# Optimization experiments

Measured on AMD Instinct MI355X. Metric: run time of the kernel, lower is better.

## Reference

```python
import jax, jax.numpy as jnp
import numpy as np

X_DIM = 512
Z_DIM = 16
HEADS = 8
DIM_HEAD = 64
INNER = HEADS * DIM_HEAD
EPS = 1e-5


def _layernorm(t, g, b):
    mu = jnp.mean(t, axis=-1, keepdims=True)
    var = jnp.mean(jnp.square(t - mu), axis=-1, keepdims=True)
    return (t - mu) * jax.lax.rsqrt(var + EPS) * g + b


def setup_inputs() -> dict:
    key = jax.random.key(0)
    ks = jax.random.split(key, 8)
    B, N = 4, 2048
    s_x = 1.0 / np.sqrt(X_DIM)
    s_z = 1.0 / np.sqrt(Z_DIM)
    s_i = 1.0 / np.sqrt(INNER)
    return {
        "x": jax.random.normal(ks[0], (B, N, X_DIM), dtype=jnp.float32),
        "z": jax.random.normal(ks[1], (B, 1, Z_DIM), dtype=jnp.float32),
        "ln_x_g": jnp.ones((X_DIM,), jnp.float32),
        "ln_x_b": jnp.zeros((X_DIM,), jnp.float32),
        "ln_z_g": jnp.ones((Z_DIM,), jnp.float32),
        "ln_z_b": jnp.zeros((Z_DIM,), jnp.float32),
        "Wq": jax.random.normal(ks[2], (X_DIM, INNER), jnp.float32) * s_x,
        "Wk": jax.random.normal(ks[3], (X_DIM, INNER), jnp.float32) * s_x,
        "Wv": jax.random.normal(ks[4], (X_DIM, INNER), jnp.float32) * s_x,
        "Wz": jax.random.normal(ks[5], (Z_DIM, 2 * X_DIM), jnp.float32) * s_z,
        "Wo": jax.random.normal(ks[6], (INNER, X_DIM), jnp.float32) * s_i,
        "bo": jnp.zeros((X_DIM,), jnp.float32),
    }


def reference(x, z, ln_x_g, ln_x_b, ln_z_g, ln_z_b, Wq, Wk, Wv, Wz, Wo, bo):
    scale = DIM_HEAD ** (-0.5)
    # z path: LN -> Linear -> SiLU -> split into FiLM scale/shift
    zp = jax.nn.silu(_layernorm(z, ln_z_g, ln_z_b) @ Wz)  # [B, 1, 2*x_dim]
    z1, z2 = jnp.split(zp, 2, axis=-1)
    x_mod = _layernorm(x, ln_x_g, ln_x_b) * z1 + z2       # [B, N, x_dim]
    B, N, _ = x.shape

    def heads(t):  # [B, N, inner] -> [B, h, N, d]
        return t.reshape(B, N, HEADS, DIM_HEAD).transpose(0, 2, 1, 3)

    q = heads(x_mod @ Wq)
    k = heads(x_mod @ Wk)
    v = heads(x_mod @ Wv)
    sim = jnp.einsum('bhid,bhjd->bhij', q, k) * scale
    attn = jax.nn.softmax(sim, axis=-1)
    out = jnp.einsum('bhij,bhjd->bhid', attn, v)           # [B, h, N, d]
    out = out.transpose(0, 2, 1, 3).reshape(B, N, INNER)
    return out @ Wo + bo
```

## Files before the change

kernel.cpp:

```cpp
#include <hip/hip_runtime.h>

#define XD 512
#define HEADS 8
#define DH 64
#define NSEQ 2048
#define NBATCH 4
#define NROWS (NBATCH*NSEQ)

#define SCALE_L2E 0.18033688011112042f
#define DEFER_THR 4.0f

typedef __attribute__((ext_vector_type(8))) short bf16x8;
typedef __attribute__((ext_vector_type(8))) unsigned short u16x8;
typedef __attribute__((ext_vector_type(4))) float f32x4;
typedef __attribute__((ext_vector_type(16))) float f32x16;

__device__ __forceinline__ unsigned short f2bf(float f) {
  union { float f; unsigned u; } v; v.f = f;
  return (unsigned short)((v.u + 0x7fffu + ((v.u >> 16) & 1u)) >> 16);
}

__device__ __forceinline__ float fexp2(float x) {
#if __has_builtin(__builtin_amdgcn_exp2f)
  return __builtin_amdgcn_exp2f(x);
#else
  return exp2f(x);
#endif
}

__device__ __forceinline__ unsigned cvt_pk_bf16(float lo, float hi) {
  unsigned r;
  asm("v_cvt_pk_bf16_f32 %0, %1, %2" : "=v"(r) : "v"(lo), "v"(hi));
  return r;
}

__device__ __forceinline__ void gload_lds16(const unsigned short* g, unsigned short* l) {
  __builtin_amdgcn_global_load_lds(
      (const __attribute__((address_space(1))) unsigned int*)g,
      (__attribute__((address_space(3))) unsigned int*)l, 16, 0, 0);
}

__global__ __launch_bounds__(256) void zpath_kernel(
    const float* __restrict__ z, const float* __restrict__ g, const float* __restrict__ b,
    const float* __restrict__ Wz, float* __restrict__ z12) {
  int bb = blockIdx.x;
  int t = threadIdx.x;
  float zv[16];
  float mean = 0.f;
#pragma unroll
  for (int i = 0; i < 16; ++i) { zv[i] = z[bb * 16 + i]; mean += zv[i]; }
  mean *= (1.f / 16.f);
  float var = 0.f;
#pragma unroll
  for (int i = 0; i < 16; ++i) { float d = zv[i] - mean; var += d * d; }
  var *= (1.f / 16.f);
  float rs = rsqrtf(var + 1e-5f);
  float zn[16];
#pragma unroll
  for (int i = 0; i < 16; ++i) zn[i] = (zv[i] - mean) * rs * g[i] + b[i];
  for (int c = t; c < 1024; c += 256) {
    float acc = 0.f;
#pragma unroll
    for (int i = 0; i < 16; ++i) acc += zn[i] * Wz[i * 1024 + c];
    float s = acc / (1.f + __expf(-acc));
    z12[bb * 1024 + c] = s;
  }
}

__global__ __launch_bounds__(256) void xmod_kernel(
    const float* __restrict__ x, const float* __restrict__ g, const float* __restrict__ b,
    const float* __restrict__ z12, unsigned short* __restrict__ xm) {
  int wave = threadIdx.x >> 6, lane = threadIdx.x & 63;
  int row = blockIdx.x * 4 + wave;
  const float* xr = x + (size_t)row * XD;
  float4 v0 = ((const float4*)xr)[lane * 2];
  float4 v1 = ((const float4*)xr)[lane * 2 + 1];
  float vv[8] = {v0.x, v0.y, v0.z, v0.w, v1.x, v1.y, v1.z, v1.w};
  float sum = 0.f, sq = 0.f;
#pragma unroll
  for (int i = 0; i < 8; ++i) { sum += vv[i]; sq += vv[i] * vv[i]; }
#pragma unroll
  for (int o = 32; o; o >>= 1) { sum += __shfl_xor(sum, o); sq += __shfl_xor(sq, o); }
  float mean = sum * (1.f / 512.f);
  float var = sq * (1.f / 512.f) - mean * mean;
  float rs = rsqrtf(var + 1e-5f);
  int bb = row >> 11;
  const float* zz = z12 + bb * 1024;
  int c0 = lane * 8;
  u16x8 o8;
#pragma unroll
  for (int i = 0; i < 8; ++i) {
    int c = c0 + i;
    float t = (vv[i] - mean) * rs * g[c] + b[c];
    t = t * zz[c] + zz[512 + c];
    o8[i] = f2bf(t);
  }
  *(u16x8*)(xm + (size_t)row * XD + c0) = o8;
}

__global__ __launch_bounds__(256) void wtrans4_kernel(
    const float* __restrict__ W0, const float* __restrict__ W1,
    const float* __restrict__ W2, const float* __restrict__ W3,
    unsigned short* __restrict__ dst) {
  __shared__ float tile[32][33];
  int blk = blockIdx.x;
  int w = blk >> 8;
  int t = blk & 255;
  int tn = t >> 4, tk = t & 15;
  const float* W = (w == 0) ? W0 : (w == 1) ? W1 : (w == 2) ? W2 : W3;
  int r = threadIdx.x >> 5, c = threadIdx.x & 31;
#pragma unroll
  for (int i = 0; i < 4; ++i)
    tile[r + 8 * i][c] = W[(size_t)(tk * 32 + r + 8 * i) * 512 + tn * 32 + c];
  __syncthreads();
  unsigned short* d = dst + (size_t)w * 262144;
#pragma unroll
  for (int i = 0; i < 4; ++i)
    d[(size_t)(tn * 32 + r + 8 * i) * 512 + tk * 32 + c] = f2bf(tile[c][r + 8 * i]);
}

__global__ __launch_bounds__(256, 2) void gemm_qkv_kernel(
    const unsigned short* __restrict__ A, const unsigned short* __restrict__ Wt,
    unsigned short* __restrict__ Qo, unsigned short* __restrict__ Ko,
    unsigned short* __restrict__ Vo) {
  __shared__ unsigned short Alds[128 * 64];
  __shared__ unsigned short Blds[128 * 64];
  int widx = threadIdx.x >> 6, lane = threadIdx.x & 63;
  int blk = blockIdx.x;
  int nt = blk % 12, mt = blk / 12;
  int blkM = mt * 128, blkN = nt * 128;
  int wr = widx >> 1, wc = widx & 1;
  int lr = lane & 15, lg = lane >> 4;
  int srow = lane >> 3, sc8 = lane & 7;

  f32x4 acc[4][4] = {};

  for (int kc = 0; kc < 512; kc += 64) {
#pragma unroll
    for (int i = 0; i < 4; ++i) {
      int rb = widx * 32 + i * 8;
      int row = rb + srow;
      int cs = (sc8 ^ (row & 7)) * 8;
      gload_lds16(A + (size_t)(blkM + row) * 512 + kc + cs, &Alds[rb * 64]);
      gload_lds16(Wt + (size_t)(blkN + row) * 512 + kc + cs, &Blds[rb * 64]);
    }
    __syncthreads();

#pragma unroll
    for (int kh = 0; kh < 2; ++kh) {
      bf16x8 bfr[4];
#pragma unroll
      for (int ni = 0; ni < 4; ++ni) {
        int brow = wc * 64 + ni * 16 + lr;
        bfr[ni] = *(const bf16x8*)&Blds[brow * 64 + (((kh * 4 + lg) ^ (brow & 7)) * 8)];
      }
#pragma unroll
      for (int mi = 0; mi < 4; ++mi) {
        int arow = wr * 64 + mi * 16 + lr;
        bf16x8 afr = *(const bf16x8*)&Alds[arow * 64 + (((kh * 4 + lg) ^ (arow & 7)) * 8)];
#pragma unroll
        for (int ni = 0; ni < 4; ++ni)
          acc[mi][ni] = __builtin_amdgcn_mfma_f32_16x16x32_bf16(afr, bfr[ni], acc[mi][ni], 0, 0, 0);
      }
    }
    __syncthreads();
  }

  int cg = blkN >> 9;
#pragma unroll
  for (int mi = 0; mi < 4; ++mi)
#pragma unroll
    for (int ni = 0; ni < 4; ++ni) {
      int col = blkN + wc * 64 + ni * 16 + lr;
      int c = col & 511;
#pragma unroll
      for (int j = 0; j < 4; ++j) {
        int row = blkM + wr * 64 + mi * 16 + lg * 4 + j;
        float v = acc[mi][ni][j];
        if (cg == 0) {
          Qo[(size_t)row * 512 + c] = f2bf(v * SCALE_L2E);
        } else if (cg == 1) {
          Ko[(size_t)row * 512 + c] = f2bf(v);
        } else {
          int bb = row >> 11, n = row & 2047, h = c >> 6, d = c & 63;
          int j4 = n & 15;
          int slot = (j4 & 3) | (((j4 >> 3) & 1) << 2) | (((j4 >> 2) & 1) << 3);
          int np = (n & ~15) | slot;
          Vo[(((size_t)(bb * HEADS + h) * DH + d) << 11) + np] = f2bf(v);
        }
      }
    }
}

__global__ __launch_bounds__(256, 2) void gemm_out_kernel(
    const unsigned short* __restrict__ A, const unsigned short* __restrict__ Wt,
    float* __restrict__ out, const float* __restrict__ bias) {
  __shared__ unsigned short Alds[128 * 64];
  __shared__ unsigned short Blds[64 * 64];
  int widx = threadIdx.x >> 6, lane = threadIdx.x & 63;
  int blk = blockIdx.x;
  int nt = blk & 7, mt = blk >> 3;
  int blkM = mt * 128, blkN = nt * 64;
  int wr = widx >> 1, wc = widx & 1;
  int lr = lane & 15, lg = lane >> 4;
  int srow = lane >> 3, sc8 = lane & 7;

  f32x4 acc[4][2] = {};

  for (int kc = 0; kc < 512; kc += 64) {
#pragma unroll
    for (int i = 0; i < 4; ++i) {
      int rb = widx * 32 + i * 8;
      int row = rb + srow;
      int cs = (sc8 ^ (row & 7)) * 8;
      gload_lds16(A + (size_t)(blkM + row) * 512 + kc + cs, &Alds[rb * 64]);
    }
#pragma unroll
    for (int i = 0; i < 2; ++i) {
      int rb = widx * 16 + i * 8;
      int row = rb + srow;
      int cs = (sc8 ^ (row & 7)) * 8;
      gload_lds16(Wt + (size_t)(blkN + row) * 512 + kc + cs, &Blds[rb * 64]);
    }
    __syncthreads();

#pragma unroll
    for (int kh = 0; kh < 2; ++kh) {
      bf16x8 bfr[2];
#pragma unroll
      for (int ni = 0; ni < 2; ++ni) {
        int brow = wc * 32 + ni * 16 + lr;
        bfr[ni] = *(const bf16x8*)&Blds[brow * 64 + (((kh * 4 + lg) ^ (brow & 7)) * 8)];
      }
#pragma unroll
      for (int mi = 0; mi < 4; ++mi) {
        int arow = wr * 64 + mi * 16 + lr;
        bf16x8 afr = *(const bf16x8*)&Alds[arow * 64 + (((kh * 4 + lg) ^ (arow & 7)) * 8)];
#pragma unroll
        for (int ni = 0; ni < 2; ++ni)
          acc[mi][ni] = __builtin_amdgcn_mfma_f32_16x16x32_bf16(afr, bfr[ni], acc[mi][ni], 0, 0, 0);
      }
    }
    __syncthreads();
  }

#pragma unroll
  for (int mi = 0; mi < 4; ++mi)
#pragma unroll
    for (int ni = 0; ni < 2; ++ni) {
      int col = blkN + wc * 32 + ni * 16 + lr;
#pragma unroll
      for (int j = 0; j < 4; ++j) {
        int row = blkM + wr * 64 + mi * 16 + lg * 4 + j;
        out[(size_t)row * 512 + col] = acc[mi][ni][j] + bias[col];
      }
    }
}


#define AKV 64
#define NCH_S 16

#define STAGE_S(s_, buf, kcc) do {                                        \
    _Pragma("unroll")                                                     \
    for (int i = 0; i < 2; ++i) {                                         \
      int rb = wq * 16 + i * 8;                                           \
      int row = rb + (lane >> 3);                                         \
      int cs = (lane & 7) ^ (row & 7);                                    \
      gload_lds16(Kg + (size_t)((kcc) + row) * 512 + cs * 8, KLDS(s_, buf) + rb * 64); \
      gload_lds16(Vg + (size_t)row * NSEQ + (kcc) + cs * 8, VLDS(s_, buf) + rb * 64);  \
    }                                                                     \
  } while (0)

#define PROCESS64(kb_, vb_) do {                                          \
    f32x16 s[2];                                                          \
    __builtin_amdgcn_s_setprio(1);                                        \
    _Pragma("unroll")                                                     \
    for (int kt = 0; kt < 2; ++kt) {                                      \
      int krow = kt * 32 + ql;                                            \
      f32x16 z = {};                                                      \
      _Pragma("unroll")                                                   \
      for (int ks = 0; ks < 4; ++ks) {                                    \
        bf16x8 kf = *(const bf16x8*)((kb_) + krow * 64 + (((ks * 2 + hi) ^ (krow & 7)) * 8)); \
        z = __builtin_amdgcn_mfma_f32_32x32x16_bf16(kf, qf[ks], z, 0, 0, 0); \
      }                                                                   \
      s[kt] = z;                                                          \
    }                                                                     \
    __builtin_amdgcn_s_setprio(0);                                        \
    float m8 = s[0][0];                                                   \
    _Pragma("unroll")                                                     \
    for (int i = 1; i < 16; ++i) m8 = fmaxf(m8, s[0][i]);                 \
    _Pragma("unroll")                                                     \
    for (int i = 0; i < 16; ++i) m8 = fmaxf(m8, s[1][i]);                 \
    m8 = fmaxf(m8, __shfl_xor(m8, 32));                                   \
    bool grow = (m8 > m0 + DEFER_THR);                                    \
    if (__any((int)grow)) {                                               \
      float mn = fmaxf(m0, m8);                                           \
      float al = fexp2(m0 - mn);                                          \
      m0 = mn; l0 *= al;                                                  \
      _Pragma("unroll")                                                   \
      for (int dt = 0; dt < 2; ++dt)                                      \
        _Pragma("unroll")                                                 \
        for (int j = 0; j < 16; ++j) o[dt][j] *= al;                      \
    }                                                                     \
    float p0[16], p1[16]; float rs = 0.f;                                 \
    _Pragma("unroll")                                                     \
    for (int i = 0; i < 16; ++i) { p0[i] = fexp2(s[0][i] - m0); rs += p0[i]; } \
    _Pragma("unroll")                                                     \
    for (int i = 0; i < 16; ++i) { p1[i] = fexp2(s[1][i] - m0); rs += p1[i]; } \
    rs += __shfl_xor(rs, 32);                                             \
    l0 += rs;                                                             \
    union { unsigned w[4]; bf16x8 v; } pf[4];                             \
    _Pragma("unroll")                                                     \
    for (int d2 = 0; d2 < 4; ++d2) {                                      \
      pf[0].w[d2] = cvt_pk_bf16(p0[2 * d2], p0[2 * d2 + 1]);              \
      pf[1].w[d2] = cvt_pk_bf16(p0[8 + 2 * d2], p0[8 + 2 * d2 + 1]);      \
      pf[2].w[d2] = cvt_pk_bf16(p1[2 * d2], p1[2 * d2 + 1]);              \
      pf[3].w[d2] = cvt_pk_bf16(p1[8 + 2 * d2], p1[8 + 2 * d2 + 1]);      \
    }                                                                     \
    __builtin_amdgcn_s_setprio(1);                                        \
    _Pragma("unroll")                                                     \
    for (int dt = 0; dt < 2; ++dt) {                                      \
      int vrow = dt * 32 + ql;                                            \
      f32x16 acc = o[dt];                                                 \
      _Pragma("unroll")                                                   \
      for (int g = 0; g < 4; ++g) {                                       \
        bf16x8 vf = *(const bf16x8*)((vb_) + vrow * 64 + (((g * 2 + hi) ^ (vrow & 7)) * 8)); \
        acc = __builtin_amdgcn_mfma_f32_32x32x16_bf16(vf, pf[g].v, acc, 0, 0, 0); \
      }                                                                   \
      o[dt] = acc;                                                        \
    }                                                                     \
    __builtin_amdgcn_s_setprio(0);                                        \
  } while (0)

__global__ __launch_bounds__(512, 4) void attn_kernel(
    const unsigned short* __restrict__ Q, const unsigned short* __restrict__ K,
    const unsigned short* __restrict__ VT, unsigned short* __restrict__ O) {
  __shared__ __align__(16) unsigned short SH[2][2][2][64 * 64];
#define KLDS(s_, bf) (&SH[0][s_][bf][0])
#define VLDS(s_, bf) (&SH[1][s_][bf][0])
  int tid = threadIdx.x;
  int widx = tid >> 6, lane = tid & 63;
  int strm = widx >> 2;
  int wq = widx & 3;
  int blk = blockIdx.x;
  int xcd = blk & 7;
  int idx = blk >> 3;
  int bh = xcd * 4 + (idx >> 4);
  int qg = idx & 15;
  int b = bh >> 3, h = bh & 7;
  int ql = lane & 31, hi = lane >> 5;
  int qrow0 = qg * 128 + wq * 32;

  bf16x8 qf[4];
  const unsigned short* Qp = Q + (size_t)(b * NSEQ + qrow0 + ql) * 512 + h * 64 + hi * 8;
#pragma unroll
  for (int ks = 0; ks < 4; ++ks) qf[ks] = *(const bf16x8*)(Qp + ks * 16);

  const unsigned short* Kg = K + (size_t)b * NSEQ * 512 + h * 64 + (size_t)strm * 1024 * 512;
  const unsigned short* Vg = VT + (size_t)bh * DH * NSEQ + strm * 1024;

  float m0 = -3.0e38f, l0 = 0.f;
  f32x16 o[2] = {};

  STAGE_S(strm, 0, 0);
  __syncthreads();
  int cur = 0;
  for (int t = 0; t < NCH_S; ++t) {
    if (t + 1 < NCH_S) STAGE_S(strm, cur ^ 1, (t + 1) * AKV);
    const unsigned short* kb_ = KLDS(strm, cur);
    const unsigned short* vb_ = VLDS(strm, cur);
    PROCESS64(kb_, vb_);
    __syncthreads();
    cur ^= 1;
  }

  float* sm = (float*)&SH[0][0][0][0];
  if (strm == 1) {
    int base = (wq * 64 + lane) * 34;
    sm[base] = m0;
    sm[base + 1] = l0;
#pragma unroll
    for (int j = 0; j < 16; ++j) { sm[base + 2 + j] = o[0][j]; sm[base + 18 + j] = o[1][j]; }
  }
  __syncthreads();
  if (strm == 0) {
    int base = (wq * 64 + lane) * 34;
    float mB = sm[base], lB = sm[base + 1];
    float mN = fmaxf(m0, mB);
    float aA = fexp2(m0 - mN), aB = fexp2(mB - mN);
    float inv = 1.f / (l0 * aA + lB * aB);
    float aAi = aA * inv, aBi = aB * inv;
    size_t rowb = (size_t)(b * NSEQ + qrow0 + ql) * 512 + h * 64 + hi * 4;
#pragma unroll
    for (int dt = 0; dt < 2; ++dt)
#pragma unroll
      for (int c = 0; c < 8; ++c) {
        float vlo = o[dt][2 * c] * aAi + sm[base + 2 + dt * 16 + 2 * c] * aBi;
        float vhi = o[dt][2 * c + 1] * aAi + sm[base + 2 + dt * 16 + 2 * c + 1] * aBi;
        unsigned w = cvt_pk_bf16(vlo, vhi);
        int d0 = dt * 32 + 8 * (c >> 1) + (c & 1) * 2;
        *(unsigned*)(O + rowb + d0) = w;
      }
  }
}

extern "C" void kernel_launch(void* const* d_in, const int* in_sizes, int n_in,
                              void* d_out, int out_size, void* d_ws, size_t ws_size,
                              hipStream_t stream) {
  const float* x   = (const float*)d_in[0];
  const float* z   = (const float*)d_in[1];
  const float* lxg = (const float*)d_in[2];
  const float* lxb = (const float*)d_in[3];
  const float* lzg = (const float*)d_in[4];
  const float* lzb = (const float*)d_in[5];
  const float* Wq  = (const float*)d_in[6];
  const float* Wk  = (const float*)d_in[7];
  const float* Wv  = (const float*)d_in[8];
  const float* Wz  = (const float*)d_in[9];
  const float* Wo  = (const float*)d_in[10];
  const float* bo  = (const float*)d_in[11];

  char* ws = (char*)d_ws;
  unsigned short* xm  = (unsigned short*)(ws);
  unsigned short* qb  = (unsigned short*)(ws + 8388608);
  unsigned short* kb  = (unsigned short*)(ws + 16777216);
  unsigned short* vt  = (unsigned short*)(ws + 25165824);
  unsigned short* ao  = (unsigned short*)(ws + 33554432);
  unsigned short* wqt = (unsigned short*)(ws + 41943040);
  unsigned short* wot = (unsigned short*)(ws + 43515904);
  float*          z12 = (float*)(ws + 44040192);

  zpath_kernel<<<NBATCH, 256, 0, stream>>>(z, lzg, lzb, Wz, z12);
  xmod_kernel<<<NROWS / 4, 256, 0, stream>>>(x, lxg, lxb, z12, xm);
  wtrans4_kernel<<<1024, 256, 0, stream>>>(Wq, Wk, Wv, Wo, wqt);
  gemm_qkv_kernel<<<768, 256, 0, stream>>>(xm, wqt, qb, kb, vt);
  attn_kernel<<<512, 512, 0, stream>>>(qb, kb, vt, ao);
  gemm_out_kernel<<<512, 256, 0, stream>>>(ao, wot, (float*)d_out, bo);
}
```

Measured before the change: 106.0 us.

## Double-buffer GEMM LDS loads, merge z-path into weight transpose, tree-reduce softmax max

```diff
diff --git a/kernel.cpp b/kernel.cpp
--- a/kernel.cpp
+++ b/kernel.cpp
@@ -40,30 +40,51 @@
       (__attribute__((address_space(3))) unsigned int*)l, 16, 0, 0);
 }
 
-__global__ __launch_bounds__(256) void zpath_kernel(
-    const float* __restrict__ z, const float* __restrict__ g, const float* __restrict__ b,
+__global__ __launch_bounds__(256) void wtrans4z_kernel(
+    const float* __restrict__ W0, const float* __restrict__ W1,
+    const float* __restrict__ W2, const float* __restrict__ W3,
+    unsigned short* __restrict__ dst,
+    const float* __restrict__ z, const float* __restrict__ zg, const float* __restrict__ zb,
     const float* __restrict__ Wz, float* __restrict__ z12) {
-  int bb = blockIdx.x;
-  int t = threadIdx.x;
-  float zv[16];
-  float mean = 0.f;
-#pragma unroll
-  for (int i = 0; i < 16; ++i) { zv[i] = z[bb * 16 + i]; mean += zv[i]; }
-  mean *= (1.f / 16.f);
-  float var = 0.f;
-#pragma unroll
-  for (int i = 0; i < 16; ++i) { float d = zv[i] - mean; var += d * d; }
-  var *= (1.f / 16.f);
-  float rs = rsqrtf(var + 1e-5f);
-  float zn[16];
-#pragma unroll
-  for (int i = 0; i < 16; ++i) zn[i] = (zv[i] - mean) * rs * g[i] + b[i];
-  for (int c = t; c < 1024; c += 256) {
-    float acc = 0.f;
-#pragma unroll
-    for (int i = 0; i < 16; ++i) acc += zn[i] * Wz[i * 1024 + c];
-    float s = acc / (1.f + __expf(-acc));
-    z12[bb * 1024 + c] = s;
+  __shared__ float tile[32][33];
+  int blk = blockIdx.x;
+  if (blk < 1024) {
+    int w = blk >> 8;
+    int t = blk & 255;
+    int tn = t >> 4, tk = t & 15;
+    const float* W = (w == 0) ? W0 : (w == 1) ? W1 : (w == 2) ? W2 : W3;
+    int r = threadIdx.x >> 5, c = threadIdx.x & 31;
+#pragma unroll
+    for (int i = 0; i < 4; ++i)
+      tile[r + 8 * i][c] = W[(size_t)(tk * 32 + r + 8 * i) * 512 + tn * 32 + c];
+    __syncthreads();
+    unsigned short* d = dst + (size_t)w * 262144;
+#pragma unroll
+    for (int i = 0; i < 4; ++i)
+      d[(size_t)(tn * 32 + r + 8 * i) * 512 + tk * 32 + c] = f2bf(tile[c][r + 8 * i]);
+  } else {
+    int bb = blk - 1024;
+    int t = threadIdx.x;
+    float zv[16];
+    float mean = 0.f;
+#pragma unroll
+    for (int i = 0; i < 16; ++i) { zv[i] = z[bb * 16 + i]; mean += zv[i]; }
+    mean *= (1.f / 16.f);
+    float var = 0.f;
+#pragma unroll
+    for (int i = 0; i < 16; ++i) { float d = zv[i] - mean; var += d * d; }
+    var *= (1.f / 16.f);
+    float rs = rsqrtf(var + 1e-5f);
+    float zn[16];
+#pragma unroll
+    for (int i = 0; i < 16; ++i) zn[i] = (zv[i] - mean) * rs * zg[i] + zb[i];
+    for (int c = t; c < 1024; c += 256) {
+      float acc = 0.f;
+#pragma unroll
+      for (int i = 0; i < 16; ++i) acc += zn[i] * Wz[i * 1024 + c];
+      float s = acc / (1.f + __expf(-acc));
+      z12[bb * 1024 + c] = s;
+    }
   }
 }
 
@@ -98,33 +119,12 @@
   *(u16x8*)(xm + (size_t)row * XD + c0) = o8;
 }
 
-__global__ __launch_bounds__(256) void wtrans4_kernel(
-    const float* __restrict__ W0, const float* __restrict__ W1,
-    const float* __restrict__ W2, const float* __restrict__ W3,
-    unsigned short* __restrict__ dst) {
-  __shared__ float tile[32][33];
-  int blk = blockIdx.x;
-  int w = blk >> 8;
-  int t = blk & 255;
-  int tn = t >> 4, tk = t & 15;
-  const float* W = (w == 0) ? W0 : (w == 1) ? W1 : (w == 2) ? W2 : W3;
-  int r = threadIdx.x >> 5, c = threadIdx.x & 31;
-#pragma unroll
-  for (int i = 0; i < 4; ++i)
-    tile[r + 8 * i][c] = W[(size_t)(tk * 32 + r + 8 * i) * 512 + tn * 32 + c];
-  __syncthreads();
-  unsigned short* d = dst + (size_t)w * 262144;
-#pragma unroll
-  for (int i = 0; i < 4; ++i)
-    d[(size_t)(tn * 32 + r + 8 * i) * 512 + tk * 32 + c] = f2bf(tile[c][r + 8 * i]);
-}
-
 __global__ __launch_bounds__(256, 2) void gemm_qkv_kernel(
     const unsigned short* __restrict__ A, const unsigned short* __restrict__ Wt,
     unsigned short* __restrict__ Qo, unsigned short* __restrict__ Ko,
     unsigned short* __restrict__ Vo) {
-  __shared__ unsigned short Alds[128 * 64];
-  __shared__ unsigned short Blds[128 * 64];
+  __shared__ unsigned short Alds[2][128 * 64];
+  __shared__ unsigned short Blds[2][128 * 64];
   int widx = threadIdx.x >> 6, lane = threadIdx.x & 63;
   int blk = blockIdx.x;
   int nt = blk % 12, mt = blk / 12;
@@ -133,18 +133,25 @@
   int lr = lane & 15, lg = lane >> 4;
   int srow = lane >> 3, sc8 = lane & 7;
 
+#define STAGEQ(bf, kcc) do {                                              \
+    _Pragma("unroll")                                                     \
+    for (int i = 0; i < 4; ++i) {                                         \
+      int rb = widx * 32 + i * 8;                                         \
+      int row = rb + srow;                                                \
+      int cs = (sc8 ^ (row & 7)) * 8;                                     \
+      gload_lds16(A + (size_t)(blkM + row) * 512 + (kcc) + cs, &Alds[bf][rb * 64]);  \
+      gload_lds16(Wt + (size_t)(blkN + row) * 512 + (kcc) + cs, &Blds[bf][rb * 64]); \
+    }                                                                     \
+  } while (0)
+
   f32x4 acc[4][4] = {};
 
+  STAGEQ(0, 0);
+  asm volatile("s_waitcnt vmcnt(0)" ::: "memory");
+  __builtin_amdgcn_s_barrier();
+  int cur = 0;
   for (int kc = 0; kc < 512; kc += 64) {
-#pragma unroll
-    for (int i = 0; i < 4; ++i) {
-      int rb = widx * 32 + i * 8;
-      int row = rb + srow;
-      int cs = (sc8 ^ (row & 7)) * 8;
-      gload_lds16(A + (size_t)(blkM + row) * 512 + kc + cs, &Alds[rb * 64]);
-      gload_lds16(Wt + (size_t)(blkN + row) * 512 + kc + cs, &Blds[rb * 64]);
-    }
-    __syncthreads();
+    if (kc + 64 < 512) STAGEQ(cur ^ 1, kc + 64);
 
 #pragma unroll
     for (int kh = 0; kh < 2; ++kh) {
@@ -152,18 +159,20 @@
 #pragma unroll
       for (int ni = 0; ni < 4; ++ni) {
         int brow = wc * 64 + ni * 16 + lr;
-        bfr[ni] = *(const bf16x8*)&Blds[brow * 64 + (((kh * 4 + lg) ^ (brow & 7)) * 8)];
+        bfr[ni] = *(const bf16x8*)&Blds[cur][brow * 64 + (((kh * 4 + lg) ^ (brow & 7)) * 8)];
       }
 #pragma unroll
       for (int mi = 0; mi < 4; ++mi) {
         int arow = wr * 64 + mi * 16 + lr;
-        bf16x8 afr = *(const bf16x8*)&Alds[arow * 64 + (((kh * 4 + lg) ^ (arow & 7)) * 8)];
+        bf16x8 afr = *(const bf16x8*)&Alds[cur][arow * 64 + (((kh * 4 + lg) ^ (arow & 7)) * 8)];
 #pragma unroll
         for (int ni = 0; ni < 4; ++ni)
           acc[mi][ni] = __builtin_amdgcn_mfma_f32_16x16x32_bf16(afr, bfr[ni], acc[mi][ni], 0, 0, 0);
       }
     }
-    __syncthreads();
+    asm volatile("s_waitcnt vmcnt(0)" ::: "memory");
+    __builtin_amdgcn_s_barrier();
+    cur ^= 1;
   }
 
   int cg = blkN >> 9;
@@ -195,8 +204,8 @@
 __global__ __launch_bounds__(256, 2) void gemm_out_kernel(
     const unsigned short* __restrict__ A, const unsigned short* __restrict__ Wt,
     float* __restrict__ out, const float* __restrict__ bias) {
-  __shared__ unsigned short Alds[128 * 64];
-  __shared__ unsigned short Blds[64 * 64];
+  __shared__ unsigned short Alds[2][128 * 64];
+  __shared__ unsigned short Blds[2][64 * 64];
   int widx = threadIdx.x >> 6, lane = threadIdx.x & 63;
   int blk = blockIdx.x;
   int nt = blk & 7, mt = blk >> 3;
@@ -205,24 +214,31 @@
   int lr = lane & 15, lg = lane >> 4;
   int srow = lane >> 3, sc8 = lane & 7;
 
+#define STAGEO(bf, kcc) do {                                              \
+    _Pragma("unroll")                                                     \
+    for (int i = 0; i < 4; ++i) {                                         \
+      int rb = widx * 32 + i * 8;                                         \
+      int row = rb + srow;                                                \
+      int cs = (sc8 ^ (row & 7)) * 8;                                     \
+      gload_lds16(A + (size_t)(blkM + row) * 512 + (kcc) + cs, &Alds[bf][rb * 64]);  \
+    }                                                                     \
+    _Pragma("unroll")                                                     \
+    for (int i = 0; i < 2; ++i) {                                         \
+      int rb = widx * 16 + i * 8;                                         \
+      int row = rb + srow;                                                \
+      int cs = (sc8 ^ (row & 7)) * 8;                                     \
+      gload_lds16(Wt + (size_t)(blkN + row) * 512 + (kcc) + cs, &Blds[bf][rb * 64]); \
+    }                                                                     \
+  } while (0)
+
   f32x4 acc[4][2] = {};
 
+  STAGEO(0, 0);
+  asm volatile("s_waitcnt vmcnt(0)" ::: "memory");
+  __builtin_amdgcn_s_barrier();
+  int cur = 0;
   for (int kc = 0; kc < 512; kc += 64) {
-#pragma unroll
-    for (int i = 0; i < 4; ++i) {
-      int rb = widx * 32 + i * 8;
-      int row = rb + srow;
-      int cs = (sc8 ^ (row & 7)) * 8;
-      gload_lds16(A + (size_t)(blkM + row) * 512 + kc + cs, &Alds[rb * 64]);
-    }
-#pragma unroll
-    for (int i = 0; i < 2; ++i) {
-      int rb = widx * 16 + i * 8;
-      int row = rb + srow;
-      int cs = (sc8 ^ (row & 7)) * 8;
-      gload_lds16(Wt + (size_t)(blkN + row) * 512 + kc + cs, &Blds[rb * 64]);
-    }
-    __syncthreads();
+    if (kc + 64 < 512) STAGEO(cur ^ 1, kc + 64);
 
 #pragma unroll
     for (int kh = 0; kh < 2; ++kh) {
@@ -230,18 +246,20 @@
 #pragma unroll
       for (int ni = 0; ni < 2; ++ni) {
         int brow = wc * 32 + ni * 16 + lr;
-        bfr[ni] = *(const bf16x8*)&Blds[brow * 64 + (((kh * 4 + lg) ^ (brow & 7)) * 8)];
+        bfr[ni] = *(const bf16x8*)&Blds[cur][brow * 64 + (((kh * 4 + lg) ^ (brow & 7)) * 8)];
       }
 #pragma unroll
       for (int mi = 0; mi < 4; ++mi) {
         int arow = wr * 64 + mi * 16 + lr;
-        bf16x8 afr = *(const bf16x8*)&Alds[arow * 64 + (((kh * 4 + lg) ^ (arow & 7)) * 8)];
+        bf16x8 afr = *(const bf16x8*)&Alds[cur][arow * 64 + (((kh * 4 + lg) ^ (arow & 7)) * 8)];
 #pragma unroll
         for (int ni = 0; ni < 2; ++ni)
           acc[mi][ni] = __builtin_amdgcn_mfma_f32_16x16x32_bf16(afr, bfr[ni], acc[mi][ni], 0, 0, 0);
       }
     }
-    __syncthreads();
+    asm volatile("s_waitcnt vmcnt(0)" ::: "memory");
+    __builtin_amdgcn_s_barrier();
+    cur ^= 1;
   }
 
 #pragma unroll
@@ -287,11 +305,13 @@
       s[kt] = z;                                                          \
     }                                                                     \
     __builtin_amdgcn_s_setprio(0);                                        \
-    float m8 = s[0][0];                                                   \
-    _Pragma("unroll")                                                     \
-    for (int i = 1; i < 16; ++i) m8 = fmaxf(m8, s[0][i]);                 \
-    _Pragma("unroll")                                                     \
-    for (int i = 0; i < 16; ++i) m8 = fmaxf(m8, s[1][i]);                 \
+                                \
+    float q4[8];                                                          \
+    _Pragma("unroll")                                                     \
+    for (int i = 0; i < 8; ++i)                                           \
+      q4[i] = fmaxf(fmaxf(s[0][i], s[0][i + 8]), fmaxf(s[1][i], s[1][i + 8])); \
+    float m8 = fmaxf(fmaxf(fmaxf(q4[0], q4[1]), fmaxf(q4[2], q4[3])),     \
+                     fmaxf(fmaxf(q4[4], q4[5]), fmaxf(q4[6], q4[7])));    \
     m8 = fmaxf(m8, __shfl_xor(m8, 32));                                   \
     bool grow = (m8 > m0 + DEFER_THR);                                    \
     if (__any((int)grow)) {                                               \
@@ -303,11 +323,12 @@
         _Pragma("unroll")                                                 \
         for (int j = 0; j < 16; ++j) o[dt][j] *= al;                      \
     }                                                                     \
-    float p0[16], p1[16]; float rs = 0.f;                                 \
-    _Pragma("unroll")                                                     \
-    for (int i = 0; i < 16; ++i) { p0[i] = fexp2(s[0][i] - m0); rs += p0[i]; } \
-    _Pragma("unroll")                                                     \
-    for (int i = 0; i < 16; ++i) { p1[i] = fexp2(s[1][i] - m0); rs += p1[i]; } \
+    float p0[16], p1[16]; float rsA = 0.f, rsB = 0.f;                     \
+    _Pragma("unroll")                                                     \
+    for (int i = 0; i < 16; ++i) { p0[i] = fexp2(s[0][i] - m0); rsA += p0[i]; } \
+    _Pragma("unroll")                                                     \
+    for (int i = 0; i < 16; ++i) { p1[i] = fexp2(s[1][i] - m0); rsB += p1[i]; } \
+    float rs = rsA + rsB;                                                 \
     rs += __shfl_xor(rs, 32);                                             \
     l0 += rs;                                                             \
     union { unsigned w[4]; bf16x8 v; } pf[4];                             \
@@ -431,9 +452,8 @@
   unsigned short* wot = (unsigned short*)(ws + 43515904);
   float*          z12 = (float*)(ws + 44040192);
 
-  zpath_kernel<<<NBATCH, 256, 0, stream>>>(z, lzg, lzb, Wz, z12);
+  wtrans4z_kernel<<<1028, 256, 0, stream>>>(Wq, Wk, Wv, Wo, wqt, z, lzg, lzb, Wz, z12);
   xmod_kernel<<<NROWS / 4, 256, 0, stream>>>(x, lxg, lxb, z12, xm);
-  wtrans4_kernel<<<1024, 256, 0, stream>>>(Wq, Wk, Wv, Wo, wqt);
   gemm_qkv_kernel<<<768, 256, 0, stream>>>(xm, wqt, qb, kb, vt);
   attn_kernel<<<512, 512, 0, stream>>>(qb, kb, vt, ao);
   gemm_out_kernel<<<512, 256, 0, stream>>>(ao, wot, (float*)d_out, bo);
```

Result: slower. 115.2 us (+8.7%).

## Merge z-path into weight transpose, remap GEMM blocks per XCD, shorten softmax reductions

Applied to the files above, without the earlier changes.

```diff
diff --git a/kernel.cpp b/kernel.cpp
--- a/kernel.cpp
+++ b/kernel.cpp
@@ -40,30 +40,51 @@
       (__attribute__((address_space(3))) unsigned int*)l, 16, 0, 0);
 }
 
-__global__ __launch_bounds__(256) void zpath_kernel(
-    const float* __restrict__ z, const float* __restrict__ g, const float* __restrict__ b,
+__global__ __launch_bounds__(256) void wtrans4z_kernel(
+    const float* __restrict__ W0, const float* __restrict__ W1,
+    const float* __restrict__ W2, const float* __restrict__ W3,
+    unsigned short* __restrict__ dst,
+    const float* __restrict__ z, const float* __restrict__ zg, const float* __restrict__ zb,
     const float* __restrict__ Wz, float* __restrict__ z12) {
-  int bb = blockIdx.x;
-  int t = threadIdx.x;
-  float zv[16];
-  float mean = 0.f;
-#pragma unroll
-  for (int i = 0; i < 16; ++i) { zv[i] = z[bb * 16 + i]; mean += zv[i]; }
-  mean *= (1.f / 16.f);
-  float var = 0.f;
-#pragma unroll
-  for (int i = 0; i < 16; ++i) { float d = zv[i] - mean; var += d * d; }
-  var *= (1.f / 16.f);
-  float rs = rsqrtf(var + 1e-5f);
-  float zn[16];
-#pragma unroll
-  for (int i = 0; i < 16; ++i) zn[i] = (zv[i] - mean) * rs * g[i] + b[i];
-  for (int c = t; c < 1024; c += 256) {
-    float acc = 0.f;
-#pragma unroll
-    for (int i = 0; i < 16; ++i) acc += zn[i] * Wz[i * 1024 + c];
-    float s = acc / (1.f + __expf(-acc));
-    z12[bb * 1024 + c] = s;
+  __shared__ float tile[32][33];
+  int blk = blockIdx.x;
+  if (blk < 1024) {
+    int w = blk >> 8;
+    int t = blk & 255;
+    int tn = t >> 4, tk = t & 15;
+    const float* W = (w == 0) ? W0 : (w == 1) ? W1 : (w == 2) ? W2 : W3;
+    int r = threadIdx.x >> 5, c = threadIdx.x & 31;
+#pragma unroll
+    for (int i = 0; i < 4; ++i)
+      tile[r + 8 * i][c] = W[(size_t)(tk * 32 + r + 8 * i) * 512 + tn * 32 + c];
+    __syncthreads();
+    unsigned short* d = dst + (size_t)w * 262144;
+#pragma unroll
+    for (int i = 0; i < 4; ++i)
+      d[(size_t)(tn * 32 + r + 8 * i) * 512 + tk * 32 + c] = f2bf(tile[c][r + 8 * i]);
+  } else {
+    int bb = blk - 1024;
+    int t = threadIdx.x;
+    float zv[16];
+    float mean = 0.f;
+#pragma unroll
+    for (int i = 0; i < 16; ++i) { zv[i] = z[bb * 16 + i]; mean += zv[i]; }
+    mean *= (1.f / 16.f);
+    float var = 0.f;
+#pragma unroll
+    for (int i = 0; i < 16; ++i) { float d = zv[i] - mean; var += d * d; }
+    var *= (1.f / 16.f);
+    float rs = rsqrtf(var + 1e-5f);
+    float zn[16];
+#pragma unroll
+    for (int i = 0; i < 16; ++i) zn[i] = (zv[i] - mean) * rs * zg[i] + zb[i];
+    for (int c = t; c < 1024; c += 256) {
+      float acc = 0.f;
+#pragma unroll
+      for (int i = 0; i < 16; ++i) acc += zn[i] * Wz[i * 1024 + c];
+      float s = acc / (1.f + __expf(-acc));
+      z12[bb * 1024 + c] = s;
+    }
   }
 }
 
@@ -98,27 +119,6 @@
   *(u16x8*)(xm + (size_t)row * XD + c0) = o8;
 }
 
-__global__ __launch_bounds__(256) void wtrans4_kernel(
-    const float* __restrict__ W0, const float* __restrict__ W1,
-    const float* __restrict__ W2, const float* __restrict__ W3,
-    unsigned short* __restrict__ dst) {
-  __shared__ float tile[32][33];
-  int blk = blockIdx.x;
-  int w = blk >> 8;
-  int t = blk & 255;
-  int tn = t >> 4, tk = t & 15;
-  const float* W = (w == 0) ? W0 : (w == 1) ? W1 : (w == 2) ? W2 : W3;
-  int r = threadIdx.x >> 5, c = threadIdx.x & 31;
-#pragma unroll
-  for (int i = 0; i < 4; ++i)
-    tile[r + 8 * i][c] = W[(size_t)(tk * 32 + r + 8 * i) * 512 + tn * 32 + c];
-  __syncthreads();
-  unsigned short* d = dst + (size_t)w * 262144;
-#pragma unroll
-  for (int i = 0; i < 4; ++i)
-    d[(size_t)(tn * 32 + r + 8 * i) * 512 + tk * 32 + c] = f2bf(tile[c][r + 8 * i]);
-}
-
 __global__ __launch_bounds__(256, 2) void gemm_qkv_kernel(
     const unsigned short* __restrict__ A, const unsigned short* __restrict__ Wt,
     unsigned short* __restrict__ Qo, unsigned short* __restrict__ Ko,
@@ -127,7 +127,9 @@
   __shared__ unsigned short Blds[128 * 64];
   int widx = threadIdx.x >> 6, lane = threadIdx.x & 63;
   int blk = blockIdx.x;
-  int nt = blk % 12, mt = blk / 12;
+  int xcd = blk & 7, local = blk >> 3;
+  int mt = xcd * 8 + local / 12;
+  int nt = local % 12;
   int blkM = mt * 128, blkN = nt * 128;
   int wr = widx >> 1, wc = widx & 1;
   int lr = lane & 15, lg = lane >> 4;
@@ -199,7 +201,9 @@
   __shared__ unsigned short Blds[64 * 64];
   int widx = threadIdx.x >> 6, lane = threadIdx.x & 63;
   int blk = blockIdx.x;
-  int nt = blk & 7, mt = blk >> 3;
+  int xcd = blk & 7, local = blk >> 3;
+  int mt = xcd * 8 + (local >> 3);
+  int nt = local & 7;
   int blkM = mt * 128, blkN = nt * 64;
   int wr = widx >> 1, wc = widx & 1;
   int lr = lane & 15, lg = lane >> 4;
@@ -287,11 +291,13 @@
       s[kt] = z;                                                          \
     }                                                                     \
     __builtin_amdgcn_s_setprio(0);                                        \
-    float m8 = s[0][0];                                                   \
-    _Pragma("unroll")                                                     \
-    for (int i = 1; i < 16; ++i) m8 = fmaxf(m8, s[0][i]);                 \
-    _Pragma("unroll")                                                     \
-    for (int i = 0; i < 16; ++i) m8 = fmaxf(m8, s[1][i]);                 \
+                                \
+    float q4[8];                                                          \
+    _Pragma("unroll")                                                     \
+    for (int i = 0; i < 8; ++i)                                           \
+      q4[i] = fmaxf(fmaxf(s[0][i], s[0][i + 8]), fmaxf(s[1][i], s[1][i + 8])); \
+    float m8 = fmaxf(fmaxf(fmaxf(q4[0], q4[1]), fmaxf(q4[2], q4[3])),     \
+                     fmaxf(fmaxf(q4[4], q4[5]), fmaxf(q4[6], q4[7])));    \
     m8 = fmaxf(m8, __shfl_xor(m8, 32));                                   \
     bool grow = (m8 > m0 + DEFER_THR);                                    \
     if (__any((int)grow)) {                                               \
@@ -303,11 +309,12 @@
         _Pragma("unroll")                                                 \
         for (int j = 0; j < 16; ++j) o[dt][j] *= al;                      \
     }                                                                     \
-    float p0[16], p1[16]; float rs = 0.f;                                 \
-    _Pragma("unroll")                                                     \
-    for (int i = 0; i < 16; ++i) { p0[i] = fexp2(s[0][i] - m0); rs += p0[i]; } \
-    _Pragma("unroll")                                                     \
-    for (int i = 0; i < 16; ++i) { p1[i] = fexp2(s[1][i] - m0); rs += p1[i]; } \
+    float p0[16], p1[16]; float rsA = 0.f, rsB = 0.f;                     \
+    _Pragma("unroll")                                                     \
+    for (int i = 0; i < 16; ++i) { p0[i] = fexp2(s[0][i] - m0); rsA += p0[i]; } \
+    _Pragma("unroll")                                                     \
+    for (int i = 0; i < 16; ++i) { p1[i] = fexp2(s[1][i] - m0); rsB += p1[i]; } \
+    float rs = rsA + rsB;                                                 \
     rs += __shfl_xor(rs, 32);                                             \
     l0 += rs;                                                             \
     union { unsigned w[4]; bf16x8 v; } pf[4];                             \
@@ -431,9 +438,8 @@
   unsigned short* wot = (unsigned short*)(ws + 43515904);
   float*          z12 = (float*)(ws + 44040192);
 
-  zpath_kernel<<<NBATCH, 256, 0, stream>>>(z, lzg, lzb, Wz, z12);
+  wtrans4z_kernel<<<1028, 256, 0, stream>>>(Wq, Wk, Wv, Wo, wqt, z, lzg, lzb, Wz, z12);
   xmod_kernel<<<NROWS / 4, 256, 0, stream>>>(x, lxg, lxb, z12, xm);
-  wtrans4_kernel<<<1024, 256, 0, stream>>>(Wq, Wk, Wv, Wo, wqt);
   gemm_qkv_kernel<<<768, 256, 0, stream>>>(xm, wqt, qb, kb, vt);
   attn_kernel<<<512, 512, 0, stream>>>(qb, kb, vt, ao);
   gemm_out_kernel<<<512, 256, 0, stream>>>(ao, wot, (float*)d_out, bo);
```

Measured after the change: 96.12 us. 1.1x faster.
